# Performance work log

Hardware: AMD Instinct MI355X
Metric: run time of the kernel (lower is better)

## Reference

```python
import jax, jax.numpy as jnp
import numpy as np

B, D, H = 16384, 1024, 4096


def setup_inputs() -> dict:
    key = jax.random.key(0)
    kx, kp, k1, k2 = jax.random.split(key, 4)
    X = jax.random.normal(kx, (B, D), dtype=jnp.float32)
    prot_col_idx = 3
    # protected column must be binary {0,1} so the remap produces no NaNs
    prot = jax.random.randint(kp, (B,), 0, 2).astype(jnp.float32)
    X = X.at[:, prot_col_idx].set(prot)
    W1 = jax.random.normal(k1, (D, H), dtype=jnp.float32) * (1.0 / np.sqrt(D))
    b1 = jnp.zeros((H,), dtype=jnp.float32)
    W2 = jax.random.normal(k2, (H, D), dtype=jnp.float32) * (1.0 / np.sqrt(H))
    b2 = jnp.zeros((D,), dtype=jnp.float32)
    return {"X": X, "W1": W1, "b1": b1, "W2": W2, "b2": b2,
            "prot_col_idx": prot_col_idx}


def reference(X, W1, b1, W2, b2, prot_col_idx):
    def explainer(x):
        h = jnp.tanh(x @ W1 + b1)          # [B, H]
        return h @ W2 + b2                  # [B, D]

    # vectorized remap of the protected column: 0 -> 1, 1 -> 0, else NaN
    col = X[:, prot_col_idx]
    flipped = jnp.where(col == 0, jnp.float32(1.0),
                        jnp.where(col == 1, jnp.float32(0.0), jnp.float32(jnp.nan)))
    X_copy = X.at[:, prot_col_idx].set(flipped.astype(X.dtype))

    shaps = explainer(X)
    shaps_counter = explainer(X_copy)
    mean_euclid_dist = jnp.mean(jnp.abs(shaps - shaps_counter), axis=0)  # [D]
    return mean_euclid_dist.sum()
```

## Files before the change

kernel.cpp:

```cpp
#include <hip/hip_runtime.h>
#include <stdint.h>

#define B_N 16384
#define D_N 1024
#define H_N 4096

typedef int i32x4 __attribute__((ext_vector_type(4)));
typedef int i32x8 __attribute__((ext_vector_type(8)));
typedef float f32x4 __attribute__((ext_vector_type(4)));

__device__ __forceinline__ void gload16(const void* g, void* l) {
  __builtin_amdgcn_global_load_lds((const __attribute__((address_space(1))) void*)g,
                                   (__attribute__((address_space(3))) void*)l,
                                   16, 0, 0);
}

__device__ __forceinline__ unsigned char f2fp8(float v) {
  return (unsigned char)(__builtin_amdgcn_cvt_pk_fp8_f32(v, v, 0, false) & 0xFF);
}

__device__ __forceinline__ int perm_h(int h) {
  return (h & ~63) | ((h & 15) << 2) | ((h >> 4) & 3);
}

__device__ __forceinline__ void transpose_tile(
    const float* __restrict__ in, unsigned char* __restrict__ out,
    int R, int C, float scale, float* __restrict__ w3, int pci,
    int i0, int j0, int tx, int ty, bool permute) {
  __shared__ float tile[32][33];
#pragma unroll
  for (int r = 0; r < 32; r += 8) {
    int i = i0 + ty + r;
    int j = j0 + tx;
    float v = in[(size_t)i * C + j];
    tile[ty + r][tx] = v;
    if (w3 != nullptr && i == pci) w3[j] = v;
  }
  __syncthreads();
#pragma unroll
  for (int r = 0; r < 32; r += 8) {
    int jo = j0 + ty + r;
    int io = i0 + tx;
    int ioo = permute ? perm_h(io) : io;
    out[(size_t)jo * R + ioo] = f2fp8(tile[tx][ty + r] * scale);
  }
}

__global__ __launch_bounds__(256) void prep_kernel(
    const float4* __restrict__ X4, int* __restrict__ Xb,
    float* __restrict__ s,
    const float* __restrict__ W1, unsigned char* __restrict__ W1T, float* __restrict__ w3,
    const float* __restrict__ W2, unsigned char* __restrict__ W2T,
    const int* __restrict__ pci_p, float* __restrict__ out0) {
  int b = blockIdx.x;
  int tid = threadIdx.x;
  int pci = *pci_p;
  if (b == 0 && tid == 0) out0[0] = 0.0f;
  if (b < 8192) {
    int i = (b * 256 + tid) * 2;
#pragma unroll
    for (int u = 0; u < 2; u++) {
      float4 v = X4[i + u];
      int p = __builtin_amdgcn_cvt_pk_fp8_f32(v.x, v.y, 0, false);
      p = __builtin_amdgcn_cvt_pk_fp8_f32(v.z, v.w, p, true);
      Xb[i + u] = p;
      if (((i + u) & (D_N / 4 - 1)) == (pci >> 2)) {
        int row = (i + u) >> 8;
        float c;
        switch (pci & 3) {
          case 0:  c = v.x; break;
          case 1:  c = v.y; break;
          case 2:  c = v.z; break;
          default: c = v.w; break;
        }
        s[row] = 1.0f - 2.0f * c;
      }
    }
  } else if (b < 12288) {
    int id = b - 8192;
    transpose_tile(W1, W1T, D_N, H_N, 16.0f, w3, pci,
                   (id >> 7) * 32, (id & 127) * 32, tid & 31, tid >> 5, false);
  } else {
    int id = b - 12288;
    transpose_tile(W2, W2T, H_N, D_N, 64.0f, nullptr, -1,
                   (id >> 5) * 32, (id & 31) * 32, tid & 31, tid >> 5, true);
  }
}

template <int KTOT>
__device__ __forceinline__ void mx8_mainloop(
    const unsigned char* __restrict__ A, const unsigned char* __restrict__ B,
    int m0, int n0, int sa, int sb,
    unsigned char* __restrict__ As, unsigned char* __restrict__ Bs,
    f32x4 (&acc)[8][4]) {
  static_assert(KTOT % 256 == 0, "need an even number of 128-K tiles");
  const int tid = threadIdx.x;
  const int lane = tid & 63;
  const int wave = tid >> 6;
  const int wm = (wave >> 2) * 128;
  const int wn = (wave & 3) * 64;
  const int lm = lane & 15;
  const int quad = lane >> 4;

  const int srow = tid >> 3;
  const int sg = tid & 7;
  const unsigned char* Ag = A + (size_t)(m0 + srow) * KTOT + ((sg ^ (srow & 7)) * 16);
  const unsigned char* Bg = B + (size_t)(n0 + srow) * KTOT + ((sg ^ (srow & 7)) * 16);
  unsigned char* AsW = As + tid * 16;
  unsigned char* BsW = Bs + tid * 16;

  const int e = lm & 7;
  const int lo_off = ((2 * quad) ^ e) * 16;
  const int hi_off = ((2 * quad + 1) ^ e) * 16;
  const unsigned char* Ard_lo = As + (wm + lm) * 128 + lo_off;
  const unsigned char* Ard_hi = As + (wm + lm) * 128 + hi_off;
  const unsigned char* Brd_lo = Bs + (wn + lm) * 128 + lo_off;
  const unsigned char* Brd_hi = Bs + (wn + lm) * 128 + hi_off;

#define STGA(c_, kn_, p_) \
    gload16(Ag + (kn_) + (size_t)(c_) * 64 * KTOT, AsW + (p_) * 32768 + (c_) * 8192)
#define STGB(c_, kn_, p_) \
    gload16(Bg + (kn_) + (size_t)(c_) * 64 * KTOT, BsW + (p_) * 32768 + (c_) * 8192)
#define LDA(d_, i_, P_) { \
    i32x4 lo_ = *(const i32x4*)(Ard_lo + (P_) * 32768 + (i_) * 2048); \
    i32x4 hi_ = *(const i32x4*)(Ard_hi + (P_) * 32768 + (i_) * 2048); \
    d_ = __builtin_shufflevector(lo_, hi_, 0, 1, 2, 3, 4, 5, 6, 7); }
#define LDB(d_, j_, P_) { \
    i32x4 lo_ = *(const i32x4*)(Brd_lo + (P_) * 32768 + (j_) * 2048); \
    i32x4 hi_ = *(const i32x4*)(Brd_hi + (P_) * 32768 + (j_) * 2048); \
    d_ = __builtin_shufflevector(lo_, hi_, 0, 1, 2, 3, 4, 5, 6, 7); }
#define MF(a_, b_, c_) \
    __builtin_amdgcn_mfma_scale_f32_16x16x128_f8f6f4((a_), (b_), (c_), 0, 0, 0, sa, 0, sb)
#define FENCE() asm volatile("" ::: "memory")
#define BARR() { FENCE(); __builtin_amdgcn_s_barrier(); FENCE(); }
#define MM8(i0_, i1_, aA_, aB_) { \
    __builtin_amdgcn_s_setprio(1); \
    acc[i0_][0] = MF(aA_, b0, acc[i0_][0]); \
    acc[i0_][1] = MF(aA_, b1, acc[i0_][1]); \
    acc[i0_][2] = MF(aA_, b2, acc[i0_][2]); \
    acc[i0_][3] = MF(aA_, b3, acc[i0_][3]); \
    acc[i1_][0] = MF(aB_, b0, acc[i1_][0]); \
    acc[i1_][1] = MF(aB_, b1, acc[i1_][1]); \
    acc[i1_][2] = MF(aB_, b2, acc[i1_][2]); \
    acc[i1_][3] = MF(aB_, b3, acc[i1_][3]); \
    __builtin_amdgcn_s_setprio(0); }

#define TILE(P_, kn_, PF_) { \
    i32x8 b0, b1, b2, b3, av0, av1; \
     \
    LDB(b0, 0, P_); LDB(b1, 1, P_); LDB(b2, 2, P_); LDB(b3, 3, P_); \
    LDA(av0, 0, P_); LDA(av1, 1, P_); \
    if (PF_) { STGB(0, kn_, 1 - (P_)); STGB(1, kn_, 1 - (P_)); } \
    BARR(); MM8(0, 1, av0, av1); BARR(); \
     \
    LDA(av0, 2, P_); LDA(av1, 3, P_); \
    if (PF_) { STGB(2, kn_, 1 - (P_)); STGB(3, kn_, 1 - (P_)); } \
    BARR(); MM8(2, 3, av0, av1); \
     \
     \
    if (PF_) { asm volatile("s_waitcnt vmcnt(4)" ::: "memory"); } \
    else     { asm volatile("s_waitcnt vmcnt(0)" ::: "memory"); } \
    BARR(); \
     \
    LDA(av0, 4, P_); LDA(av1, 5, P_); \
    if (PF_) { STGA(0, kn_, 1 - (P_)); STGA(2, kn_, 1 - (P_)); } \
    BARR(); MM8(4, 5, av0, av1); BARR(); \
     \
    LDA(av0, 6, P_); LDA(av1, 7, P_); \
    if (PF_) { STGA(1, kn_, 1 - (P_)); STGA(3, kn_, 1 - (P_)); } \
    BARR(); MM8(6, 7, av0, av1); \
     \
    if (PF_) { asm volatile("s_waitcnt vmcnt(2)" ::: "memory"); } \
    BARR(); }

  STGB(0, 0, 0); STGB(1, 0, 0); STGB(2, 0, 0); STGB(3, 0, 0);
  STGA(0, 0, 0); STGA(2, 0, 0);
  STGA(1, 0, 0); STGA(3, 0, 0);
  asm volatile("s_waitcnt vmcnt(2)" ::: "memory");
  BARR();

  const int NT = KTOT / 128;
  for (int t = 0; t < NT - 2; t += 2) {
    TILE(0, (t + 1) * 128, true);
    TILE(1, (t + 2) * 128, true);
  }
  TILE(0, (NT - 1) * 128, true);
  TILE(1, 0, false);

#undef STGA
#undef STGB
#undef LDA
#undef LDB
#undef MF
#undef FENCE
#undef BARR
#undef MM8
#undef TILE
}

__global__ __launch_bounds__(512, 2) void gemm1_dh(
    const unsigned char* __restrict__ Xb,
    const unsigned char* __restrict__ W1T,
    const float* __restrict__ b1,
    const float* __restrict__ w3,
    const float* __restrict__ s,
    unsigned int* __restrict__ Dh4) {
  __shared__ alignas(16) unsigned char As[65536];
  __shared__ alignas(16) unsigned char Bs[65536];
  const int l = blockIdx.x;
  const int x = l & 7;
  const int k = l >> 3;
  const int m0 = (x * 8 + (k & 7)) * 256;
  const int n0 = (k >> 3) * 256;

  f32x4 acc[8][4] = {};
  mx8_mainloop<D_N>(Xb, W1T, m0, n0, 127, 123, As, Bs, acc);

  const int tid = threadIdx.x;
  const int lane = tid & 63;
  const int wave = tid >> 6;
  const int wm = (wave >> 2) * 128;
  const int wn = (wave & 3) * 64;
  const int lm = lane & 15;
  const int quad = lane >> 4;

  float ewp[4], ewm[4], nump[4], numm[4], b1v[4];
#pragma unroll
  for (int j = 0; j < 4; j++) {
    int gh = n0 + wn + j * 16 + lm;
    float w = w3[gh];
    float ep = __expf(2.0f * w);
    float em = __expf(-2.0f * w);
    ewp[j] = ep; ewm[j] = em;
    nump[j] = 128.0f * (1.0f - ep);
    numm[j] = 128.0f * (1.0f - em);
    b1v[j] = b1[gh];
  }
  const size_t coloff = (size_t)((n0 + wn) >> 2) + lm;
#pragma unroll
  for (int i = 0; i < 8; i++) {
#pragma unroll
    for (int r = 0; r < 4; r++) {
      int gb = m0 + wm + i * 16 + quad * 4 + r;
      bool sp = s[gb] > 0.0f;
      float o[4];
#pragma unroll
      for (int j = 0; j < 4; j++) {
        float ews = sp ? ewp[j] : ewm[j];
        float num = sp ? nump[j] : numm[j];
        float z = fminf(acc[i][j][r] + b1v[j], 12.0f);
        float E = __expf(2.0f * z);
        float den = (E * ews + 1.0f) * (E + 1.0f);
        o[j] = (E * num) * __builtin_amdgcn_rcpf(den);
      }
      int p = __builtin_amdgcn_cvt_pk_fp8_f32(o[0], o[1], 0, false);
      p = __builtin_amdgcn_cvt_pk_fp8_f32(o[2], o[3], p, true);
      Dh4[(size_t)gb * (H_N / 4) + coloff] = (unsigned int)p;
    }
  }
}

__global__ __launch_bounds__(512, 2) void gemm2_abs(
    const unsigned char* __restrict__ Dh,
    const unsigned char* __restrict__ W2T,
    float* __restrict__ out) {
  __shared__ alignas(16) unsigned char As[65536];
  __shared__ alignas(16) unsigned char Bs[65536];
  __shared__ float wsum[8];
  const int l = blockIdx.x;
  const int x = l & 7;
  const int k = l >> 3;
  const int m0 = (x * 8 + (k & 7)) * 256;
  const int n0 = (k >> 3) * 256;

  f32x4 acc[8][4] = {};
  mx8_mainloop<H_N>(Dh, W2T, m0, n0, 121, 121, As, Bs, acc);

  const int tid = threadIdx.x;
  const int lane = tid & 63;
  const int wave = tid >> 6;

  float t = 0.0f;
#pragma unroll
  for (int i = 0; i < 8; i++)
#pragma unroll
    for (int j = 0; j < 4; j++)
#pragma unroll
      for (int r = 0; r < 4; r++)
        t += fabsf(acc[i][j][r]);

#pragma unroll
  for (int off2 = 32; off2 > 0; off2 >>= 1)
    t += __shfl_down(t, off2, 64);
  if (lane == 0) wsum[wave] = t;
  __syncthreads();
  if (tid == 0) {
    float tt = 0.0f;
#pragma unroll
    for (int w = 0; w < 8; w++) tt += wsum[w];
    atomicAdd(out, tt * (1.0f / (float)B_N));
  }
}

extern "C" void kernel_launch(void* const* d_in, const int* in_sizes, int n_in,
                              void* d_out, int out_size, void* d_ws, size_t ws_size,
                              hipStream_t stream) {
  const float* X  = (const float*)d_in[0];
  const float* W1 = (const float*)d_in[1];
  const float* b1 = (const float*)d_in[2];
  const float* W2 = (const float*)d_in[3];
  const int* pci  = (const int*)d_in[5];

  char* ws = (char*)d_ws;
  size_t off = 0;
  unsigned char* Xb  = (unsigned char*)(ws + off); off += (size_t)B_N * D_N;
  unsigned char* W1T = (unsigned char*)(ws + off); off += (size_t)H_N * D_N;
  unsigned char* W2T = (unsigned char*)(ws + off); off += (size_t)D_N * H_N;
  float* w3  = (float*)(ws + off); off += (size_t)H_N * 4;
  float* s   = (float*)(ws + off); off += (size_t)B_N * 4;
  unsigned char* Dh  = (unsigned char*)(ws + off); off += (size_t)B_N * H_N;
  if (ws_size < off) return;

  prep_kernel<<<16384, 256, 0, stream>>>((const float4*)X, (int*)Xb, s,
                                         W1, W1T, w3, W2, W2T, pci,
                                         (float*)d_out);
  gemm1_dh<<<1024, 512, 0, stream>>>(Xb, W1T, b1, w3, s, (unsigned int*)Dh);
  gemm2_abs<<<256, 512, 0, stream>>>(Dh, W2T, (float*)d_out);
}
```

Before: 289.6 us.

## Software-pipeline LDS fragment loads one MFMA group ahead across tiles

Restructures the FP8 MFMA main loop so each group of LDS reads (A and B fragments) is issued before the preceding group of MFMAs rather than right before its own. B fragments for the next tile are preloaded into ping-pong register sets at the end of the current tile. The change also removes several barriers, merges global-to-LDS prefetch issues, and adds sched_barrier fences to hold the ordering. The aim is to hide LDS latency behind MFMA work and cut barrier stalls, at the cost of extra live registers under launch_bounds(512,2), which may cause spills.

```diff
diff --git a/kernel.cpp b/kernel.cpp
--- a/kernel.cpp
+++ b/kernel.cpp
@@ -117,6 +117,9 @@
   const unsigned char* Brd_lo = Bs + (wn + lm) * 128 + lo_off;
   const unsigned char* Brd_hi = Bs + (wn + lm) * 128 + hi_off;
 
+  i32x8 bA0, bA1, bA2, bA3, bB0, bB1, bB2, bB3;
+  i32x8 ax0, ax1, ay0, ay1;
+
 #define STGA(c_, kn_, p_) \
     gload16(Ag + (kn_) + (size_t)(c_) * 64 * KTOT, AsW + (p_) * 32768 + (c_) * 8192)
 #define STGB(c_, kn_, p_) \
@@ -131,69 +134,79 @@
     d_ = __builtin_shufflevector(lo_, hi_, 0, 1, 2, 3, 4, 5, 6, 7); }
 #define MF(a_, b_, c_) \
     __builtin_amdgcn_mfma_scale_f32_16x16x128_f8f6f4((a_), (b_), (c_), 0, 0, 0, sa, 0, sb)
-#define FENCE() asm volatile("" ::: "memory")
-#define BARR() { FENCE(); __builtin_amdgcn_s_barrier(); FENCE(); }
-#define MM8(i0_, i1_, aA_, aB_) { \
+#define BARR() { asm volatile("" ::: "memory"); __builtin_amdgcn_s_barrier(); \
+                 asm volatile("" ::: "memory"); }
+#define VM(n_) asm volatile("s_waitcnt vmcnt(" #n_ ")" ::: "memory")
+#define SCHED0() __builtin_amdgcn_sched_barrier(0)
+#define MM8(i0_, i1_, aA_, aB_, B0_, B1_, B2_, B3_) { \
     __builtin_amdgcn_s_setprio(1); \
-    acc[i0_][0] = MF(aA_, b0, acc[i0_][0]); \
-    acc[i0_][1] = MF(aA_, b1, acc[i0_][1]); \
-    acc[i0_][2] = MF(aA_, b2, acc[i0_][2]); \
-    acc[i0_][3] = MF(aA_, b3, acc[i0_][3]); \
-    acc[i1_][0] = MF(aB_, b0, acc[i1_][0]); \
-    acc[i1_][1] = MF(aB_, b1, acc[i1_][1]); \
-    acc[i1_][2] = MF(aB_, b2, acc[i1_][2]); \
-    acc[i1_][3] = MF(aB_, b3, acc[i1_][3]); \
+    acc[i0_][0] = MF(aA_, B0_, acc[i0_][0]); \
+    acc[i0_][1] = MF(aA_, B1_, acc[i0_][1]); \
+    acc[i0_][2] = MF(aA_, B2_, acc[i0_][2]); \
+    acc[i0_][3] = MF(aA_, B3_, acc[i0_][3]); \
+    acc[i1_][0] = MF(aB_, B0_, acc[i1_][0]); \
+    acc[i1_][1] = MF(aB_, B1_, acc[i1_][1]); \
+    acc[i1_][2] = MF(aB_, B2_, acc[i1_][2]); \
+    acc[i1_][3] = MF(aB_, B3_, acc[i1_][3]); \
     __builtin_amdgcn_s_setprio(0); }
 
-#define TILE(P_, kn_, PF_) { \
-    i32x8 b0, b1, b2, b3, av0, av1; \
+#define TILE(P_, BC0_, BC1_, BC2_, BC3_, BN0_, BN1_, BN2_, BN3_, kn_, LAST_) { \
      \
-    LDB(b0, 0, P_); LDB(b1, 1, P_); LDB(b2, 2, P_); LDB(b3, 3, P_); \
-    LDA(av0, 0, P_); LDA(av1, 1, P_); \
-    if (PF_) { STGB(0, kn_, 1 - (P_)); STGB(1, kn_, 1 - (P_)); } \
-    BARR(); MM8(0, 1, av0, av1); BARR(); \
-     \
-    LDA(av0, 2, P_); LDA(av1, 3, P_); \
-    if (PF_) { STGB(2, kn_, 1 - (P_)); STGB(3, kn_, 1 - (P_)); } \
-    BARR(); MM8(2, 3, av0, av1); \
-     \
-     \
-    if (PF_) { asm volatile("s_waitcnt vmcnt(4)" ::: "memory"); } \
-    else     { asm volatile("s_waitcnt vmcnt(0)" ::: "memory"); } \
+    LDA(ay0, 2, P_); LDA(ay1, 3, P_); \
+    if (!(LAST_)) { STGB(0, kn_, 1 - (P_)); STGB(1, kn_, 1 - (P_)); } \
+    SCHED0(); \
+    MM8(0, 1, ax0, ax1, BC0_, BC1_, BC2_, BC3_); \
+    if (LAST_) { VM(0); } else { VM(2); }   \
     BARR(); \
      \
-    LDA(av0, 4, P_); LDA(av1, 5, P_); \
-    if (PF_) { STGA(0, kn_, 1 - (P_)); STGA(2, kn_, 1 - (P_)); } \
-    BARR(); MM8(4, 5, av0, av1); BARR(); \
+    LDA(ax0, 4, P_); LDA(ax1, 5, P_); \
+    if (!(LAST_)) { STGB(2, kn_, 1 - (P_)); STGB(3, kn_, 1 - (P_)); \
+                    STGA(0, kn_, 1 - (P_)); STGA(2, kn_, 1 - (P_)); } \
+    SCHED0(); \
+    MM8(2, 3, ay0, ay1, BC0_, BC1_, BC2_, BC3_); \
+    BARR(); \
      \
-    LDA(av0, 6, P_); LDA(av1, 7, P_); \
-    if (PF_) { STGA(1, kn_, 1 - (P_)); STGA(3, kn_, 1 - (P_)); } \
-    BARR(); MM8(6, 7, av0, av1); \
+    LDA(ay0, 6, P_); LDA(ay1, 7, P_); \
+    if (!(LAST_)) { STGA(1, kn_, 1 - (P_)); STGA(3, kn_, 1 - (P_)); } \
+    SCHED0(); \
+    MM8(4, 5, ax0, ax1, BC0_, BC1_, BC2_, BC3_); \
+    if (!(LAST_)) { VM(2); }   \
+    BARR(); \
      \
-    if (PF_) { asm volatile("s_waitcnt vmcnt(2)" ::: "memory"); } \
-    BARR(); }
+    if (!(LAST_)) { \
+      LDB(BN0_, 0, 1 - (P_)); LDB(BN1_, 1, 1 - (P_)); \
+      LDB(BN2_, 2, 1 - (P_)); LDB(BN3_, 3, 1 - (P_)); \
+      LDA(ax0, 0, 1 - (P_)); LDA(ax1, 1, 1 - (P_)); \
+    } \
+    SCHED0(); \
+    MM8(6, 7, ay0, ay1, BC0_, BC1_, BC2_, BC3_); \
+    if (!(LAST_)) { BARR(); } \
+  }
 
   STGB(0, 0, 0); STGB(1, 0, 0); STGB(2, 0, 0); STGB(3, 0, 0);
   STGA(0, 0, 0); STGA(2, 0, 0);
   STGA(1, 0, 0); STGA(3, 0, 0);
-  asm volatile("s_waitcnt vmcnt(2)" ::: "memory");
+  VM(2);
   BARR();
+  LDB(bA0, 0, 0); LDB(bA1, 1, 0); LDB(bA2, 2, 0); LDB(bA3, 3, 0);
+  LDA(ax0, 0, 0); LDA(ax1, 1, 0);
 
   const int NT = KTOT / 128;
   for (int t = 0; t < NT - 2; t += 2) {
-    TILE(0, (t + 1) * 128, true);
-    TILE(1, (t + 2) * 128, true);
-  }
-  TILE(0, (NT - 1) * 128, true);
-  TILE(1, 0, false);
+    TILE(0, bA0, bA1, bA2, bA3, bB0, bB1, bB2, bB3, (t + 1) * 128, false);
+    TILE(1, bB0, bB1, bB2, bB3, bA0, bA1, bA2, bA3, (t + 2) * 128, false);
+  }
+  TILE(0, bA0, bA1, bA2, bA3, bB0, bB1, bB2, bB3, (NT - 1) * 128, false);
+  TILE(1, bB0, bB1, bB2, bB3, bA0, bA1, bA2, bA3, 0, true);
 
 #undef STGA
 #undef STGB
 #undef LDA
 #undef LDB
 #undef MF
-#undef FENCE
 #undef BARR
+#undef VM
+#undef SCHED0
 #undef MM8
 #undef TILE
 }
```

After: 275.3 us. 1.05x faster.

## Replace interleaved barrier-heavy GEMM tile schedule with simple double-buffered stage/compute loop

Applied to the files above, without the earlier changes.

The GEMM main loop drops the fine-grained schedule that interleaved LDS reads, partial global-to-LDS prefetches and MFMA groups between many barriers, and that used s_setprio. Each half-iteration now issues the whole next-tile prefetch up front, runs all 32 MFMAs for the current buffer, then waits on vmcnt(0) and synchronises with a single barrier. A sched_barrier keeps the prefetch ahead of the compute, and the loop is no longer unrolled. This cuts barrier count and code size, but it gives up the staggered memory/compute overlap and wave-priority tricks, so latency may be exposed at each full vmcnt(0) wait.

```diff
diff --git a/kernel.cpp b/kernel.cpp
--- a/kernel.cpp
+++ b/kernel.cpp
@@ -121,6 +121,9 @@
     gload16(Ag + (kn_) + (size_t)(c_) * 64 * KTOT, AsW + (p_) * 32768 + (c_) * 8192)
 #define STGB(c_, kn_, p_) \
     gload16(Bg + (kn_) + (size_t)(c_) * 64 * KTOT, BsW + (p_) * 32768 + (c_) * 8192)
+#define STAGE(p_, kn_) { \
+    STGB(0, kn_, p_); STGB(1, kn_, p_); STGB(2, kn_, p_); STGB(3, kn_, p_); \
+    STGA(0, kn_, p_); STGA(1, kn_, p_); STGA(2, kn_, p_); STGA(3, kn_, p_); }
 #define LDA(d_, i_, P_) { \
     i32x4 lo_ = *(const i32x4*)(Ard_lo + (P_) * 32768 + (i_) * 2048); \
     i32x4 hi_ = *(const i32x4*)(Ard_hi + (P_) * 32768 + (i_) * 2048); \
@@ -131,71 +134,52 @@
     d_ = __builtin_shufflevector(lo_, hi_, 0, 1, 2, 3, 4, 5, 6, 7); }
 #define MF(a_, b_, c_) \
     __builtin_amdgcn_mfma_scale_f32_16x16x128_f8f6f4((a_), (b_), (c_), 0, 0, 0, sa, 0, sb)
-#define FENCE() asm volatile("" ::: "memory")
-#define BARR() { FENCE(); __builtin_amdgcn_s_barrier(); FENCE(); }
-#define MM8(i0_, i1_, aA_, aB_) { \
-    __builtin_amdgcn_s_setprio(1); \
-    acc[i0_][0] = MF(aA_, b0, acc[i0_][0]); \
-    acc[i0_][1] = MF(aA_, b1, acc[i0_][1]); \
-    acc[i0_][2] = MF(aA_, b2, acc[i0_][2]); \
-    acc[i0_][3] = MF(aA_, b3, acc[i0_][3]); \
-    acc[i1_][0] = MF(aB_, b0, acc[i1_][0]); \
-    acc[i1_][1] = MF(aB_, b1, acc[i1_][1]); \
-    acc[i1_][2] = MF(aB_, b2, acc[i1_][2]); \
-    acc[i1_][3] = MF(aB_, b3, acc[i1_][3]); \
-    __builtin_amdgcn_s_setprio(0); }
-
-#define TILE(P_, kn_, PF_) { \
-    i32x8 b0, b1, b2, b3, av0, av1; \
-     \
+#define BARR() { asm volatile("" ::: "memory"); __builtin_amdgcn_s_barrier(); \
+                 asm volatile("" ::: "memory"); }
+#define VM0() asm volatile("s_waitcnt vmcnt(0)" ::: "memory")
+#define SCHED0() __builtin_amdgcn_sched_barrier(0)
+#define STEP(i_, P_) { \
+    i32x8 av; LDA(av, i_, P_); \
+    acc[i_][0] = MF(av, b0, acc[i_][0]); \
+    acc[i_][1] = MF(av, b1, acc[i_][1]); \
+    acc[i_][2] = MF(av, b2, acc[i_][2]); \
+    acc[i_][3] = MF(av, b3, acc[i_][3]); }
+#define COMPUTE(P_) { \
+    i32x8 b0, b1, b2, b3; \
     LDB(b0, 0, P_); LDB(b1, 1, P_); LDB(b2, 2, P_); LDB(b3, 3, P_); \
-    LDA(av0, 0, P_); LDA(av1, 1, P_); \
-    if (PF_) { STGB(0, kn_, 1 - (P_)); STGB(1, kn_, 1 - (P_)); } \
-    BARR(); MM8(0, 1, av0, av1); BARR(); \
-     \
-    LDA(av0, 2, P_); LDA(av1, 3, P_); \
-    if (PF_) { STGB(2, kn_, 1 - (P_)); STGB(3, kn_, 1 - (P_)); } \
-    BARR(); MM8(2, 3, av0, av1); \
-     \
-     \
-    if (PF_) { asm volatile("s_waitcnt vmcnt(4)" ::: "memory"); } \
-    else     { asm volatile("s_waitcnt vmcnt(0)" ::: "memory"); } \
-    BARR(); \
-     \
-    LDA(av0, 4, P_); LDA(av1, 5, P_); \
-    if (PF_) { STGA(0, kn_, 1 - (P_)); STGA(2, kn_, 1 - (P_)); } \
-    BARR(); MM8(4, 5, av0, av1); BARR(); \
-     \
-    LDA(av0, 6, P_); LDA(av1, 7, P_); \
-    if (PF_) { STGA(1, kn_, 1 - (P_)); STGA(3, kn_, 1 - (P_)); } \
-    BARR(); MM8(6, 7, av0, av1); \
-     \
-    if (PF_) { asm volatile("s_waitcnt vmcnt(2)" ::: "memory"); } \
-    BARR(); }
-
-  STGB(0, 0, 0); STGB(1, 0, 0); STGB(2, 0, 0); STGB(3, 0, 0);
-  STGA(0, 0, 0); STGA(2, 0, 0);
-  STGA(1, 0, 0); STGA(3, 0, 0);
-  asm volatile("s_waitcnt vmcnt(2)" ::: "memory");
+    STEP(0, P_); STEP(1, P_); STEP(2, P_); STEP(3, P_); \
+    STEP(4, P_); STEP(5, P_); STEP(6, P_); STEP(7, P_); }
+
+  STAGE(0, 0);
+  VM0();
   BARR();
 
   const int NT = KTOT / 128;
-  for (int t = 0; t < NT - 2; t += 2) {
-    TILE(0, (t + 1) * 128, true);
-    TILE(1, (t + 2) * 128, true);
-  }
-  TILE(0, (NT - 1) * 128, true);
-  TILE(1, 0, false);
+#pragma unroll 1
+  for (int t = 0; t < NT; t += 2) {
+    STAGE(1, (t + 1) * 128);
+    SCHED0();
+    COMPUTE(0);
+    VM0();
+    BARR();
+    if (t + 2 < NT) { STAGE(0, (t + 2) * 128); }
+    SCHED0();
+    COMPUTE(1);
+    VM0();
+    BARR();
+  }
 
 #undef STGA
 #undef STGB
+#undef STAGE
 #undef LDA
 #undef LDB
 #undef MF
-#undef FENCE
 #undef BARR
-#undef MM8
-#undef TILE
+#undef VM0
+#undef SCHED0
+#undef STEP
+#undef COMPUTE
 }
 
 __global__ __launch_bounds__(512, 2) void gemm1_dh(
```

After: 285.7 us. Within noise of the previous version (-1.4%).
